# Optimization experiments

Hardware: AMD Instinct MI355X
Metric: run time of the kernel (lower is better)

Reference implementation:

```python
import jax, jax.numpy as jnp
import numpy as np

N_NODES = 50000
N_EDGES = 800000
D_IN = 96
D_HID = 96
D_OUT = 4


def _glorot(key, shape):
    lim = float(np.sqrt(6.0 / (shape[0] + shape[1])))
    return jax.random.uniform(key, shape, jnp.float32, -lim, lim)


def setup_inputs() -> dict:
    key = jax.random.key(0)
    ks = jax.random.split(key, 8)
    x = jax.random.normal(ks[0], (N_NODES, D_IN), jnp.float32)
    edge_index = jax.random.randint(ks[1], (2, N_EDGES), 0, N_NODES, jnp.int64)
    return {
        'x': x,
        'edge_index': edge_index,
        'W0': _glorot(ks[2], (D_IN, D_HID)), 'b0': jnp.zeros((D_HID,), jnp.float32),
        'W1': _glorot(ks[3], (D_HID, D_HID)), 'b1': jnp.zeros((D_HID,), jnp.float32),
        'W2': _glorot(ks[4], (D_HID, D_HID)), 'b2': jnp.zeros((D_HID,), jnp.float32),
        'Wfc': _glorot(ks[5], (D_HID, D_OUT)), 'bfc': jnp.zeros((D_OUT,), jnp.float32),
    }


def _gcn_conv(x, src, dst, W, b, n):
    # GCNConv: linear transform, add self-loops, symmetric degree norm, scatter-add.
    h = x @ W                                   # [N, D]
    loops = jnp.arange(n, dtype=src.dtype)
    s = jnp.concatenate([src, loops])           # [E+N]
    d = jnp.concatenate([dst, loops])
    deg = jax.ops.segment_sum(jnp.ones_like(d, dtype=h.dtype), d, num_segments=n)
    dinv = jnp.where(deg > 0, jax.lax.rsqrt(deg), 0.0)
    norm = dinv[s] * dinv[d]                    # [E+N]
    msgs = h[s] * norm[:, None]                 # gather + scale
    out = jax.ops.segment_sum(msgs, d, num_segments=n)  # scatter-add
    return out + b


def reference(x, edge_index, W0, b0, W1, b1, W2, b2, Wfc, bfc):
    src, dst = edge_index[0], edge_index[1]
    n = x.shape[0]
    h = jax.nn.relu(_gcn_conv(x, src, dst, W0, b0, n))   # dropout = identity (eval)
    h = jax.nn.relu(_gcn_conv(h, src, dst, W1, b1, n))
    h = jax.nn.relu(_gcn_conv(h, src, dst, W2, b2, n))
    return h @ Wfc + bfc
```

## Files before the change

kernel.cpp:

```cpp
#include <hip/hip_runtime.h>

typedef __bf16 bf16x8 __attribute__((ext_vector_type(8)));
typedef float  f32x4  __attribute__((ext_vector_type(4)));
typedef float  f32x8  __attribute__((ext_vector_type(8)));
typedef unsigned short ushort;
typedef ushort us8 __attribute__((ext_vector_type(8)));

constexpr int N_NODES = 50000;
constexpr int N_EDGES = 800000;
constexpr int SLOTS = 64;
constexpr int GE = N_EDGES / 256;
constexpr int WBLK = (3 * 9216) / 256;

__device__ inline float h16f(ushort u) {
    union { _Float16 h; ushort u; } cv; cv.u = u; return (float)cv.h;
}
__device__ inline ushort f16b(float f) {
    union { _Float16 h; ushort u; } cv; cv.h = (_Float16)f; return cv.u;
}
__device__ inline ushort bf16b(float f) {
    union { __bf16 b; ushort u; } cv; cv.b = (__bf16)f; return cv.u;
}

__global__ __launch_bounds__(256) void k_count(const int* __restrict__ dst,
                                               int* __restrict__ cnt,
                                               ushort* __restrict__ rank,
                                               const float* __restrict__ W0,
                                               const float* __restrict__ W1,
                                               const float* __restrict__ W2,
                                               ushort* __restrict__ Wt) {
    const int b = blockIdx.x;
    if (b < GE) {
        int e = b * 256 + threadIdx.x;
        rank[e] = (ushort)atomicAdd(&cnt[dst[e]], 1);
    } else {
        int i = (b - GE) * 256 + threadIdx.x;
        int m = i / 9216, li = i - m * 9216;
        const float* W = (m == 0) ? W0 : (m == 1) ? W1 : W2;
        int k = li / 96, c = li - k * 96;
        Wt[m * 9216 + c * 96 + k] = bf16b(W[li]);
    }
}

__global__ __launch_bounds__(256) void k_fill(const int* __restrict__ src,
                                              const int* __restrict__ dst,
                                              const int* __restrict__ cnt,
                                              const ushort* __restrict__ rank,
                                              unsigned int* __restrict__ csr) {
    int e = blockIdx.x * 256 + threadIdx.x;
    int s = src[e], d = dst[e];
    float hs = rsqrtf((float)(cnt[s] + 1));
    unsigned int entry = (unsigned int)(ushort)s | ((unsigned int)f16b(hs) << 16);
    csr[(size_t)d * SLOTS + rank[e]] = entry;
}

template<int IN>
__global__ __launch_bounds__(256) void k_gemm_mfma(const void* Xv, const ushort* __restrict__ Wt,
                                                   ushort* __restrict__ Y, int nrows) {
    __shared__ ushort sX[64 * 96];
    __shared__ ushort sW[96 * 96];
    const int tid = threadIdx.x;
    const int rowbase = blockIdx.x * 64;

    for (int i = tid; i < 96 * 96 / 8; i += 256)
        ((uint4*)sW)[i] = ((const uint4*)Wt)[i];

    if (IN == 0) {
        const float* X = (const float*)Xv;
        for (int i = tid; i < 64 * 24; i += 256) {
            int r = i / 24, c4 = i % 24;
            int gr = rowbase + r;
            float4 v = make_float4(0.f, 0.f, 0.f, 0.f);
            if (gr < nrows) v = ((const float4*)(X + (size_t)gr * 96))[c4];
            ushort* p = sX + r * 96 + c4 * 4;
            p[0] = bf16b(v.x); p[1] = bf16b(v.y); p[2] = bf16b(v.z); p[3] = bf16b(v.w);
        }
    } else {
        const ushort* X = (const ushort*)Xv;
        for (int i = tid; i < 64 * 12; i += 256) {
            int r = i / 12, c8 = i % 12;
            int gr = rowbase + r;
            uint4 v = make_uint4(0, 0, 0, 0);
            if (gr < nrows) v = ((const uint4*)(X + (size_t)gr * 96))[c8];
            ((uint4*)(sX + r * 96))[c8] = v;
        }
    }
    __syncthreads();

    const int wv = tid >> 6, lane = tid & 63, quad = lane >> 4, l16 = lane & 15;
    f32x4 acc[6];
#pragma unroll
    for (int t = 0; t < 6; ++t) acc[t] = (f32x4){0.f, 0.f, 0.f, 0.f};

    const ushort* ax = sX + (wv * 16 + l16) * 96 + quad * 8;
#pragma unroll
    for (int s = 0; s < 3; ++s) {
        bf16x8 a = *(const bf16x8*)(ax + s * 32);
#pragma unroll
        for (int t = 0; t < 6; ++t) {
            bf16x8 b = *(const bf16x8*)(sW + (t * 16 + l16) * 96 + s * 32 + quad * 8);
            acc[t] = __builtin_amdgcn_mfma_f32_16x16x32_bf16(a, b, acc[t], 0, 0, 0);
        }
    }
    const int r0 = rowbase + wv * 16 + quad * 4;
#pragma unroll
    for (int t = 0; t < 6; ++t) {
#pragma unroll
        for (int g = 0; g < 4; ++g) {
            int r = r0 + g;
            if (r < nrows) Y[(size_t)r * 96 + t * 16 + l16] = bf16b(acc[t][g]);
        }
    }
}

__device__ inline f32x8 bf8_to_f32(us8 u) {
    f32x8 r;
#pragma unroll
    for (int i = 0; i < 8; ++i) r[i] = __uint_as_float(((unsigned int)u[i]) << 16);
    return r;
}

template<int MODE>
__global__ __launch_bounds__(192) void k_agg(const ushort* __restrict__ A,
                                             const int* __restrict__ cnt,
                                             const unsigned int* __restrict__ csr,
                                             const float* __restrict__ bias,
                                             ushort* __restrict__ Hout,
                                             float* __restrict__ out4,
                                             const float* __restrict__ Wfc,
                                             const float* __restrict__ bfc) {
    __shared__ float sWfc[384];
    __shared__ float red[16][12][4];
    const int tid = threadIdx.x;
    if (MODE == 1) {
        for (int i = tid; i < 384; i += 192) sWfc[i] = Wfc[i];
        __syncthreads();
    }
    const int g = tid / 12, c = tid % 12;
    const int n = blockIdx.x * 16 + g;

    const int deg = cnt[n];
    const float dn = rsqrtf((float)(deg + 1));
    us8 a0 = *(const us8*)(A + (size_t)n * 96 + c * 8);
    f32x8 acc = bf8_to_f32(a0) * (dn * dn);

    const unsigned int* row = csr + (size_t)n * SLOTS;
    int j = 0;
    for (; j + 4 <= deg; j += 4) {
        const uint4 q = *(const uint4*)(row + j);
        const us8 u0 = *(const us8*)(A + (size_t)(q.x & 0xFFFFu) * 96 + c * 8);
        const us8 u1 = *(const us8*)(A + (size_t)(q.y & 0xFFFFu) * 96 + c * 8);
        const us8 u2 = *(const us8*)(A + (size_t)(q.z & 0xFFFFu) * 96 + c * 8);
        const us8 u3 = *(const us8*)(A + (size_t)(q.w & 0xFFFFu) * 96 + c * 8);
        acc += bf8_to_f32(u0) * (h16f((ushort)(q.x >> 16)) * dn);
        acc += bf8_to_f32(u1) * (h16f((ushort)(q.y >> 16)) * dn);
        acc += bf8_to_f32(u2) * (h16f((ushort)(q.z >> 16)) * dn);
        acc += bf8_to_f32(u3) * (h16f((ushort)(q.w >> 16)) * dn);
    }
    for (; j < deg; ++j) {
        const unsigned int e = row[j];
        const float w = h16f((ushort)(e >> 16)) * dn;
        const us8 u = *(const us8*)(A + (size_t)(e & 0xFFFFu) * 96 + c * 8);
        acc += bf8_to_f32(u) * w;
    }
#pragma unroll
    for (int f = 0; f < 8; ++f) acc[f] = fmaxf(acc[f] + bias[c * 8 + f], 0.0f);

    if (MODE == 0) {
        us8 o;
#pragma unroll
        for (int f = 0; f < 8; ++f) o[f] = bf16b(acc[f]);
        *(us8*)(Hout + (size_t)n * 96 + c * 8) = o;
    } else {
        float p0 = 0.f, p1 = 0.f, p2 = 0.f, p3 = 0.f;
#pragma unroll
        for (int f = 0; f < 8; ++f) {
            const float* wr = sWfc + (c * 8 + f) * 4;
            p0 += acc[f] * wr[0];
            p1 += acc[f] * wr[1];
            p2 += acc[f] * wr[2];
            p3 += acc[f] * wr[3];
        }
        red[g][c][0] = p0; red[g][c][1] = p1; red[g][c][2] = p2; red[g][c][3] = p3;
        __syncthreads();
        if (tid < 64) {
            const int gg = tid >> 2, jj = tid & 3;
            float s = bfc[jj];
#pragma unroll
            for (int cc = 0; cc < 12; ++cc) s += red[gg][cc][jj];
            out4[(size_t)(blockIdx.x * 16 + gg) * 4 + jj] = s;
        }
    }
}

extern "C" void kernel_launch(void* const* d_in, const int* in_sizes, int n_in,
                              void* d_out, int out_size, void* d_ws, size_t ws_size,
                              hipStream_t stream) {
    const float* x   = (const float*)d_in[0];
    const int*   ei  = (const int*)d_in[1];
    const int*   src = ei;
    const int*   dst = ei + N_EDGES;
    const float* W0  = (const float*)d_in[2];
    const float* b0  = (const float*)d_in[3];
    const float* W1  = (const float*)d_in[4];
    const float* b1  = (const float*)d_in[5];
    const float* W2  = (const float*)d_in[6];
    const float* b2  = (const float*)d_in[7];
    const float* Wfc = (const float*)d_in[8];
    const float* bfc = (const float*)d_in[9];
    float* out = (float*)d_out;

    char* w = (char*)d_ws;
    unsigned int* csr = (unsigned int*)w;  w += ((size_t)N_NODES * SLOTS * 4 + 15) & ~15ULL;
    int*    cnt  = (int*)w;                w += ((size_t)N_NODES * 4 + 15) & ~15ULL;
    ushort* rank = (ushort*)w;             w += ((size_t)N_EDGES * 2 + 15) & ~15ULL;
    ushort* Wt   = (ushort*)w;             w += ((size_t)3 * 9216 * 2 + 15) & ~15ULL;
    ushort* H    = (ushort*)w;             w += ((size_t)N_NODES * 96 * 2 + 15) & ~15ULL;
    ushort* G    = (ushort*)w;

    const int gMf  = (N_NODES + 63) / 64;
    const int gAgg = N_NODES / 16;

    hipMemsetAsync(cnt, 0, (size_t)N_NODES * 4, stream);
    hipLaunchKernelGGL(k_count, dim3(GE + WBLK), dim3(256), 0, stream,
                       dst, cnt, rank, W0, W1, W2, Wt);
    hipLaunchKernelGGL(k_fill,  dim3(GE), dim3(256), 0, stream,
                       src, dst, cnt, rank, csr);

    hipLaunchKernelGGL((k_gemm_mfma<0>), dim3(gMf), dim3(256), 0, stream,
                       (const void*)x, Wt, H, N_NODES);
    hipLaunchKernelGGL((k_agg<0>), dim3(gAgg), dim3(192), 0, stream,
                       H, cnt, csr, b0, G, (float*)nullptr,
                       (const float*)nullptr, (const float*)nullptr);
    hipLaunchKernelGGL((k_gemm_mfma<1>), dim3(gMf), dim3(256), 0, stream,
                       (const void*)G, Wt + 9216, H, N_NODES);
    hipLaunchKernelGGL((k_agg<0>), dim3(gAgg), dim3(192), 0, stream,
                       H, cnt, csr, b1, G, (float*)nullptr,
                       (const float*)nullptr, (const float*)nullptr);
    hipLaunchKernelGGL((k_gemm_mfma<1>), dim3(gMf), dim3(256), 0, stream,
                       (const void*)G, Wt + 2 * 9216, H, N_NODES);
    hipLaunchKernelGGL((k_agg<1>), dim3(gAgg), dim3(192), 0, stream,
                       H, cnt, csr, b2, (ushort*)nullptr, out, Wfc, bfc);
}
```

Baseline: 243.6 us.

## Fuse all GCN stages into one cooperative persistent kernel with grid syncs

Replaces the memset and eight separate kernel launches with a single cooperative persistent kernel. Stages are separated by grid-wide barriers, and blocks loop over virtual block indices. CSR fill is overlapped with the first GEMM in the same phase. This removes launch gaps and per-kernel tail effects, at the cost of grid-sync overhead, fixed occupancy (4 blocks/CU, 256 threads, so a quarter of threads idle in the aggregation phases), and shared memory reused across stages.

Result: slower. 697.3 us (+186.2%).

```diff
diff --git a/kernel.cpp b/kernel.cpp
--- a/kernel.cpp
+++ b/kernel.cpp
@@ -1,4 +1,7 @@
 #include <hip/hip_runtime.h>
+#include <hip/hip_cooperative_groups.h>
+
+namespace cg = cooperative_groups;
 
 typedef __bf16 bf16x8 __attribute__((ext_vector_type(8)));
 typedef float  f32x4  __attribute__((ext_vector_type(4)));
@@ -9,8 +12,10 @@
 constexpr int N_NODES = 50000;
 constexpr int N_EDGES = 800000;
 constexpr int SLOTS = 64;
-constexpr int GE = N_EDGES / 256;
+constexpr int GE   = N_EDGES / 256;
 constexpr int WBLK = (3 * 9216) / 256;
+constexpr int GMF  = (N_NODES + 63) / 64;
+constexpr int GAGG = N_NODES / 16;
 
 __device__ inline float h16f(ushort u) {
     union { _Float16 h; ushort u; } cv; cv.u = u; return (float)cv.h;
@@ -21,48 +26,24 @@
 __device__ inline ushort bf16b(float f) {
     union { __bf16 b; ushort u; } cv; cv.b = (__bf16)f; return cv.u;
 }
-
-__global__ __launch_bounds__(256) void k_count(const int* __restrict__ dst,
-                                               int* __restrict__ cnt,
-                                               ushort* __restrict__ rank,
-                                               const float* __restrict__ W0,
-                                               const float* __restrict__ W1,
-                                               const float* __restrict__ W2,
-                                               ushort* __restrict__ Wt) {
-    const int b = blockIdx.x;
-    if (b < GE) {
-        int e = b * 256 + threadIdx.x;
-        rank[e] = (ushort)atomicAdd(&cnt[dst[e]], 1);
-    } else {
-        int i = (b - GE) * 256 + threadIdx.x;
-        int m = i / 9216, li = i - m * 9216;
-        const float* W = (m == 0) ? W0 : (m == 1) ? W1 : W2;
-        int k = li / 96, c = li - k * 96;
-        Wt[m * 9216 + c * 96 + k] = bf16b(W[li]);
-    }
-}
-
-__global__ __launch_bounds__(256) void k_fill(const int* __restrict__ src,
-                                              const int* __restrict__ dst,
-                                              const int* __restrict__ cnt,
-                                              const ushort* __restrict__ rank,
-                                              unsigned int* __restrict__ csr) {
-    int e = blockIdx.x * 256 + threadIdx.x;
-    int s = src[e], d = dst[e];
-    float hs = rsqrtf((float)(cnt[s] + 1));
-    unsigned int entry = (unsigned int)(ushort)s | ((unsigned int)f16b(hs) << 16);
-    csr[(size_t)d * SLOTS + rank[e]] = entry;
+__device__ inline f32x8 bf8_to_f32(us8 u) {
+    f32x8 r;
+#pragma unroll
+    for (int i = 0; i < 8; ++i) r[i] = __uint_as_float(((unsigned int)u[i]) << 16);
+    return r;
 }
 
 template<int IN>
-__global__ __launch_bounds__(256) void k_gemm_mfma(const void* Xv, const ushort* __restrict__ Wt,
-                                                   ushort* __restrict__ Y, int nrows) {
-    __shared__ ushort sX[64 * 96];
-    __shared__ ushort sW[96 * 96];
+__device__ __forceinline__ void gemm_tile(ushort* sS, const void* Xv,
+                                          const ushort* __restrict__ Wt,
+                                          ushort* __restrict__ Y, int bt) {
+    ushort* sX = sS;
+    ushort* sW = sS + 64 * 96;
     const int tid = threadIdx.x;
-    const int rowbase = blockIdx.x * 64;
-
-    for (int i = tid; i < 96 * 96 / 8; i += 256)
+    const int rowbase = bt * 64;
+
+    __syncthreads();
+    for (int i = tid; i < 9216 / 8; i += 256)
         ((uint4*)sW)[i] = ((const uint4*)Wt)[i];
 
     if (IN == 0) {
@@ -71,7 +52,7 @@
             int r = i / 24, c4 = i % 24;
             int gr = rowbase + r;
             float4 v = make_float4(0.f, 0.f, 0.f, 0.f);
-            if (gr < nrows) v = ((const float4*)(X + (size_t)gr * 96))[c4];
+            if (gr < N_NODES) v = ((const float4*)(X + (size_t)gr * 96))[c4];
             ushort* p = sX + r * 96 + c4 * 4;
             p[0] = bf16b(v.x); p[1] = bf16b(v.y); p[2] = bf16b(v.z); p[3] = bf16b(v.w);
         }
@@ -81,7 +62,7 @@
             int r = i / 12, c8 = i % 12;
             int gr = rowbase + r;
             uint4 v = make_uint4(0, 0, 0, 0);
-            if (gr < nrows) v = ((const uint4*)(X + (size_t)gr * 96))[c8];
+            if (gr < N_NODES) v = ((const uint4*)(X + (size_t)gr * 96))[c8];
             ((uint4*)(sX + r * 96))[c8] = v;
         }
     }
@@ -108,41 +89,19 @@
 #pragma unroll
         for (int g = 0; g < 4; ++g) {
             int r = r0 + g;
-            if (r < nrows) Y[(size_t)r * 96 + t * 16 + l16] = bf16b(acc[t][g]);
-        }
-    }
-}
-
-__device__ inline f32x8 bf8_to_f32(us8 u) {
-    f32x8 r;
-#pragma unroll
-    for (int i = 0; i < 8; ++i) r[i] = __uint_as_float(((unsigned int)u[i]) << 16);
-    return r;
-}
-
-template<int MODE>
-__global__ __launch_bounds__(192) void k_agg(const ushort* __restrict__ A,
-                                             const int* __restrict__ cnt,
-                                             const unsigned int* __restrict__ csr,
-                                             const float* __restrict__ bias,
-                                             ushort* __restrict__ Hout,
-                                             float* __restrict__ out4,
-                                             const float* __restrict__ Wfc,
-                                             const float* __restrict__ bfc) {
-    __shared__ float sWfc[384];
-    __shared__ float red[16][12][4];
-    const int tid = threadIdx.x;
-    if (MODE == 1) {
-        for (int i = tid; i < 384; i += 192) sWfc[i] = Wfc[i];
-        __syncthreads();
-    }
-    const int g = tid / 12, c = tid % 12;
-    const int n = blockIdx.x * 16 + g;
-
+            if (r < N_NODES) Y[(size_t)r * 96 + t * 16 + l16] = bf16b(acc[t][g]);
+        }
+    }
+}
+
+__device__ __forceinline__ f32x8 agg_gather(const ushort* __restrict__ A,
+                                            const int* __restrict__ cnt,
+                                            const unsigned int* __restrict__ csr,
+                                            const float* __restrict__ bias,
+                                            int n, int c) {
     const int deg = cnt[n];
     const float dn = rsqrtf((float)(deg + 1));
-    us8 a0 = *(const us8*)(A + (size_t)n * 96 + c * 8);
-    f32x8 acc = bf8_to_f32(a0) * (dn * dn);
+    f32x8 acc = bf8_to_f32(*(const us8*)(A + (size_t)n * 96 + c * 8)) * (dn * dn);
 
     const unsigned int* row = csr + (size_t)n * SLOTS;
     int j = 0;
@@ -165,30 +124,118 @@
     }
 #pragma unroll
     for (int f = 0; f < 8; ++f) acc[f] = fmaxf(acc[f] + bias[c * 8 + f], 0.0f);
-
-    if (MODE == 0) {
-        us8 o;
-#pragma unroll
-        for (int f = 0; f < 8; ++f) o[f] = bf16b(acc[f]);
-        *(us8*)(Hout + (size_t)n * 96 + c * 8) = o;
-    } else {
-        float p0 = 0.f, p1 = 0.f, p2 = 0.f, p3 = 0.f;
-#pragma unroll
-        for (int f = 0; f < 8; ++f) {
-            const float* wr = sWfc + (c * 8 + f) * 4;
-            p0 += acc[f] * wr[0];
-            p1 += acc[f] * wr[1];
-            p2 += acc[f] * wr[2];
-            p3 += acc[f] * wr[3];
-        }
-        red[g][c][0] = p0; red[g][c][1] = p1; red[g][c][2] = p2; red[g][c][3] = p3;
+    return acc;
+}
+
+__global__ __launch_bounds__(256, 4) void k_mega(
+    const float* __restrict__ x, const int* __restrict__ src, const int* __restrict__ dst,
+    const float* __restrict__ W0, const float* __restrict__ W1, const float* __restrict__ W2,
+    const float* __restrict__ b0, const float* __restrict__ b1, const float* __restrict__ b2,
+    const float* __restrict__ Wfc, const float* __restrict__ bfc,
+    int* __restrict__ cnt, ushort* __restrict__ rank, unsigned int* __restrict__ csr,
+    ushort* __restrict__ Wt, ushort* __restrict__ H, ushort* __restrict__ G,
+    float* __restrict__ out) {
+    cg::grid_group grid = cg::this_grid();
+    __shared__ ushort sS[64 * 96 + 96 * 96];
+    const int tid = threadIdx.x;
+    const int GS = gridDim.x;
+
+    for (int i = blockIdx.x * 256 + tid; i < N_NODES; i += GS * 256) cnt[i] = 0;
+    grid.sync();
+
+    for (int vb = blockIdx.x; vb < GE + WBLK; vb += GS) {
+        if (vb < GE) {
+            int e = vb * 256 + tid;
+            rank[e] = (ushort)atomicAdd(&cnt[dst[e]], 1);
+        } else {
+            int i = (vb - GE) * 256 + tid;
+            int m = i / 9216, li = i - m * 9216;
+            const float* W = (m == 0) ? W0 : (m == 1) ? W1 : W2;
+            int k = li / 96, c = li - k * 96;
+            Wt[m * 9216 + c * 96 + k] = bf16b(W[li]);
+        }
+    }
+    grid.sync();
+
+    for (int vb = blockIdx.x; vb < GE + GMF; vb += GS) {
+        if (vb < GE) {
+            int e = vb * 256 + tid;
+            int s = src[e], d = dst[e];
+            float hs = rsqrtf((float)(cnt[s] + 1));
+            unsigned int entry = (unsigned int)(ushort)s | ((unsigned int)f16b(hs) << 16);
+            csr[(size_t)d * SLOTS + rank[e]] = entry;
+        } else {
+            gemm_tile<0>(sS, (const void*)x, Wt, H, vb - GE);
+        }
+    }
+    grid.sync();
+
+    for (int vb = blockIdx.x; vb < GAGG; vb += GS) {
+        if (tid < 192) {
+            int g = tid / 12, c = tid % 12;
+            int n = vb * 16 + g;
+            f32x8 acc = agg_gather(H, cnt, csr, b0, n, c);
+            us8 o;
+#pragma unroll
+            for (int f = 0; f < 8; ++f) o[f] = bf16b(acc[f]);
+            *(us8*)(G + (size_t)n * 96 + c * 8) = o;
+        }
+    }
+    grid.sync();
+
+    for (int vb = blockIdx.x; vb < GMF; vb += GS)
+        gemm_tile<1>(sS, (const void*)G, Wt + 9216, H, vb);
+    grid.sync();
+
+    for (int vb = blockIdx.x; vb < GAGG; vb += GS) {
+        if (tid < 192) {
+            int g = tid / 12, c = tid % 12;
+            int n = vb * 16 + g;
+            f32x8 acc = agg_gather(H, cnt, csr, b1, n, c);
+            us8 o;
+#pragma unroll
+            for (int f = 0; f < 8; ++f) o[f] = bf16b(acc[f]);
+            *(us8*)(G + (size_t)n * 96 + c * 8) = o;
+        }
+    }
+    grid.sync();
+
+    for (int vb = blockIdx.x; vb < GMF; vb += GS)
+        gemm_tile<1>(sS, (const void*)G, Wt + 2 * 9216, H, vb);
+    grid.sync();
+
+    {
+        float* sWfc = (float*)sS;
+        float* red  = (float*)sS + 384;
         __syncthreads();
-        if (tid < 64) {
-            const int gg = tid >> 2, jj = tid & 3;
-            float s = bfc[jj];
-#pragma unroll
-            for (int cc = 0; cc < 12; ++cc) s += red[gg][cc][jj];
-            out4[(size_t)(blockIdx.x * 16 + gg) * 4 + jj] = s;
+        for (int i = tid; i < 384; i += 256) sWfc[i] = Wfc[i];
+        __syncthreads();
+        for (int vb = blockIdx.x; vb < GAGG; vb += GS) {
+            if (tid < 192) {
+                int g = tid / 12, c = tid % 12;
+                int n = vb * 16 + g;
+                f32x8 acc = agg_gather(H, cnt, csr, b2, n, c);
+                float p0 = 0.f, p1 = 0.f, p2 = 0.f, p3 = 0.f;
+#pragma unroll
+                for (int f = 0; f < 8; ++f) {
+                    const float* wr = sWfc + (c * 8 + f) * 4;
+                    p0 += acc[f] * wr[0];
+                    p1 += acc[f] * wr[1];
+                    p2 += acc[f] * wr[2];
+                    p3 += acc[f] * wr[3];
+                }
+                float* rr = red + (g * 12 + c) * 4;
+                rr[0] = p0; rr[1] = p1; rr[2] = p2; rr[3] = p3;
+            }
+            __syncthreads();
+            if (tid < 64) {
+                int gg = tid >> 2, jj = tid & 3;
+                float s = bfc[jj];
+#pragma unroll
+                for (int cc = 0; cc < 12; ++cc) s += red[(gg * 12 + cc) * 4 + jj];
+                out[(size_t)(vb * 16 + gg) * 4 + jj] = s;
+            }
+            __syncthreads();
         }
     }
 }
@@ -218,27 +265,19 @@
     ushort* H    = (ushort*)w;             w += ((size_t)N_NODES * 96 * 2 + 15) & ~15ULL;
     ushort* G    = (ushort*)w;
 
-    const int gMf  = (N_NODES + 63) / 64;
-    const int gAgg = N_NODES / 16;
-
-    hipMemsetAsync(cnt, 0, (size_t)N_NODES * 4, stream);
-    hipLaunchKernelGGL(k_count, dim3(GE + WBLK), dim3(256), 0, stream,
-                       dst, cnt, rank, W0, W1, W2, Wt);
-    hipLaunchKernelGGL(k_fill,  dim3(GE), dim3(256), 0, stream,
-                       src, dst, cnt, rank, csr);
-
-    hipLaunchKernelGGL((k_gemm_mfma<0>), dim3(gMf), dim3(256), 0, stream,
-                       (const void*)x, Wt, H, N_NODES);
-    hipLaunchKernelGGL((k_agg<0>), dim3(gAgg), dim3(192), 0, stream,
-                       H, cnt, csr, b0, G, (float*)nullptr,
-                       (const float*)nullptr, (const float*)nullptr);
-    hipLaunchKernelGGL((k_gemm_mfma<1>), dim3(gMf), dim3(256), 0, stream,
-                       (const void*)G, Wt + 9216, H, N_NODES);
-    hipLaunchKernelGGL((k_agg<0>), dim3(gAgg), dim3(192), 0, stream,
-                       H, cnt, csr, b1, G, (float*)nullptr,
-                       (const float*)nullptr, (const float*)nullptr);
-    hipLaunchKernelGGL((k_gemm_mfma<1>), dim3(gMf), dim3(256), 0, stream,
-                       (const void*)G, Wt + 2 * 9216, H, N_NODES);
-    hipLaunchKernelGGL((k_agg<1>), dim3(gAgg), dim3(192), 0, stream,
-                       H, cnt, csr, b2, (ushort*)nullptr, out, Wfc, bfc);
-}
+    int perCU = 0;
+    hipOccupancyMaxActiveBlocksPerMultiprocessor(&perCU, (const void*)k_mega, 256, 0);
+    if (perCU < 1) perCU = 1;
+    if (perCU > 4) perCU = 4;
+    int grid = perCU * 256;
+
+    void* args[] = {
+        (void*)&x, (void*)&src, (void*)&dst,
+        (void*)&W0, (void*)&W1, (void*)&W2,
+        (void*)&b0, (void*)&b1, (void*)&b2,
+        (void*)&Wfc, (void*)&bfc,
+        (void*)&cnt, (void*)&rank, (void*)&csr,
+        (void*)&Wt, (void*)&H, (void*)&G, (void*)&out
+    };
+    hipLaunchCooperativeKernel((void*)k_mega, dim3(grid), dim3(256), args, 0, stream);
+}
```
